# Kernel optimization log

Hardware: AMD Instinct MI355X
Metric: run time of the kernel (lower is better)

Reference implementation:

```python
import jax, jax.numpy as jnp
import numpy as np

D, H, L, V, BS = 1024, 16, 12, 50257, 2048
HD = D // H
EPS = 1e-5


def _ln(x, w, b):
    m = jnp.mean(x, -1, keepdims=True)
    v = jnp.mean(jnp.square(x - m), -1, keepdims=True)
    return (x - m) * jax.lax.rsqrt(v + EPS) * w + b


def setup_inputs() -> dict:
    key = jax.random.key(0)
    ks = jax.random.split(key, 10)
    B, T = 4, 1024
    s = 0.02
    return {
        "idx": jax.random.randint(ks[0], (B, T), 0, V),
        "targets": jax.random.randint(ks[1], (B, T), 0, V),
        "wte": s * jax.random.normal(ks[2], (V, D), jnp.float32),
        "wpe": s * jax.random.normal(ks[3], (BS, D), jnp.float32),
        "ln1_w": jnp.ones((L, D), jnp.float32),
        "ln1_b": jnp.zeros((L, D), jnp.float32),
        "qkv_w": s * jax.random.normal(ks[4], (L, D, 3 * D), jnp.float32),
        "qkv_b": jnp.zeros((L, 3 * D), jnp.float32),
        "o_w": s * jax.random.normal(ks[5], (L, D, D), jnp.float32),
        "o_b": jnp.zeros((L, D), jnp.float32),
        "ln2_w": jnp.ones((L, D), jnp.float32),
        "ln2_b": jnp.zeros((L, D), jnp.float32),
        "up_w": s * jax.random.normal(ks[6], (L, D, 4 * D), jnp.float32),
        "up_b": jnp.zeros((L, 4 * D), jnp.float32),
        "down_w": s * jax.random.normal(ks[7], (L, 4 * D, D), jnp.float32),
        "down_b": jnp.zeros((L, D), jnp.float32),
        "lnf_w": jnp.ones((D,), jnp.float32),
        "lnf_b": jnp.zeros((D,), jnp.float32),
        "lm_b": jnp.zeros((V,), jnp.float32),
    }


def _gpt(idx, targets, wte, wpe, ln1_w, ln1_b, qkv_w, qkv_b, o_w, o_b,
         ln2_w, ln2_b, up_w, up_b, down_w, down_b, lnf_w, lnf_b, lm_b):
    B, T = idx.shape
    x = wte[idx] + wpe[:T][None, :, :]  # [B,T,D]
    causal = jnp.tril(jnp.ones((T, T), bool))
    scale = HD ** -0.5

    def block(h, p):
        (l1w, l1b, qw, qb, ow, ob, l2w, l2b, uw, ub, dw, db) = p
        y = _ln(h, l1w, l1b)
        qkv = y @ qw + qb  # [B,T,3D]
        q, k, v = jnp.split(qkv, 3, axis=-1)
        q = q.reshape(B, T, H, HD)
        k = k.reshape(B, T, H, HD)
        v = v.reshape(B, T, H, HD)
        scores = jnp.einsum('bqhd,bkhd->bhqk', q, k) * scale
        scores = jnp.where(causal, scores, -jnp.inf)
        attn = jax.nn.softmax(scores, axis=-1)
        o = jnp.einsum('bhqk,bkhd->bqhd', attn, v).reshape(B, T, D)
        h = h + o @ ow + ob
        y = _ln(h, l2w, l2b)
        y = jax.nn.gelu(y @ uw + ub, approximate=False)
        h = h + y @ dw + db
        return h, None

    params = (ln1_w, ln1_b, qkv_w, qkv_b, o_w, o_b, ln2_w, ln2_b, up_w, up_b, down_w, down_b)
    x, _ = jax.lax.scan(block, x, params)
    x = _ln(x, lnf_w, lnf_b)
    logits = x @ wte.T + lm_b  # tied lm_head weight
    logp = jax.nn.log_softmax(logits, axis=-1)
    nll = -jnp.take_along_axis(logp, targets[..., None], axis=-1)[..., 0]
    loss = jnp.mean(nll)
    return logits, loss


def reference(idx, targets, wte, wpe, ln1_w, ln1_b, qkv_w, qkv_b, o_w, o_b,
              ln2_w, ln2_b, up_w, up_b, down_w, down_b, lnf_w, lnf_b, lm_b):
    return _gpt(idx, targets, wte, wpe, ln1_w, ln1_b, qkv_w, qkv_b, o_w, o_b,
                ln2_w, ln2_b, up_w, up_b, down_w, down_b, lnf_w, lnf_b, lm_b)
```

## Files before the change

### kernel.cpp

```cpp
#include <hip/hip_runtime.h>
#include <hip/hip_bf16.h>
#include <math.h>

typedef __attribute__((ext_vector_type(8))) short bfrag;
typedef __attribute__((ext_vector_type(4))) float f32x4;

static constexpr int Dm = 1024, Hh = 16, HD = 64, Ll = 12, Tt = 1024, Bb = 4;
static constexpr int Vv = 50257, Mrows = 4096;
static constexpr int PLD = 200;

__device__ inline unsigned short f2bf(float f) {
    unsigned u = __float_as_uint(f);
    u += 0x7fffu + ((u >> 16) & 1u);
    return (unsigned short)(u >> 16);
}
__device__ inline float bf2f(unsigned short s) {
    return __uint_as_float(((unsigned)s) << 16);
}

__device__ inline void gload16(const unsigned short* g, unsigned short* l) {
    __builtin_amdgcn_global_load_lds(
        (const __attribute__((address_space(1))) void*)g,
        (__attribute__((address_space(3))) void*)l, 16, 0, 0);
}

__global__ __launch_bounds__(256)
void embed_kernel(float* __restrict__ x, const float* __restrict__ wte,
                  const float* __restrict__ wpe, const int* __restrict__ idx) {
    int row = blockIdx.x;
    int t = row & (Tt - 1);
    int id = idx[row];
    int c = threadIdx.x * 4;
    float4 a = *reinterpret_cast<const float4*>(&wte[(size_t)id * Dm + c]);
    float4 p = *reinterpret_cast<const float4*>(&wpe[(size_t)t * Dm + c]);
    float4 o;
    o.x = a.x + p.x; o.y = a.y + p.y; o.z = a.z + p.z; o.w = a.w + p.w;
    *reinterpret_cast<float4*>(&x[(size_t)row * Dm + c]) = o;
}

__global__ __launch_bounds__(256)
void ln_kernel(unsigned short* __restrict__ y, const float* __restrict__ x,
               const float* __restrict__ w, const float* __restrict__ b) {
    int row = blockIdx.x;
    int tid = threadIdx.x;
    int lane = tid & 63, wv = tid >> 6;
    const float* xr = x + (size_t)row * Dm;
    float4 v = *reinterpret_cast<const float4*>(&xr[tid * 4]);
    float s1 = v.x + v.y + v.z + v.w;
    float s2 = v.x * v.x + v.y * v.y + v.z * v.z + v.w * v.w;
#pragma unroll
    for (int off = 1; off < 64; off <<= 1) {
        s1 += __shfl_xor(s1, off);
        s2 += __shfl_xor(s2, off);
    }
    __shared__ float r1[4], r2[4];
    if (lane == 0) { r1[wv] = s1; r2[wv] = s2; }
    __syncthreads();
    s1 = r1[0] + r1[1] + r1[2] + r1[3];
    s2 = r2[0] + r2[1] + r2[2] + r2[3];
    float mean = s1 * (1.0f / Dm);
    float var = s2 * (1.0f / Dm) - mean * mean;
    float rstd = rsqrtf(var + 1e-5f);
    float4 wvv = *reinterpret_cast<const float4*>(&w[tid * 4]);
    float4 bv = *reinterpret_cast<const float4*>(&b[tid * 4]);
    ushort4 o;
    o.x = f2bf((v.x - mean) * rstd * wvv.x + bv.x);
    o.y = f2bf((v.y - mean) * rstd * wvv.y + bv.y);
    o.z = f2bf((v.z - mean) * rstd * wvv.z + bv.z);
    o.w = f2bf((v.w - mean) * rstd * wvv.w + bv.w);
    *reinterpret_cast<ushort4*>(&y[(size_t)row * Dm + tid * 4]) = o;
}

__global__ __launch_bounds__(256)
void transpose_layer(const float* __restrict__ qw, const float* __restrict__ ow,
                     const float* __restrict__ uw, const float* __restrict__ dw,
                     unsigned short* __restrict__ wTq, unsigned short* __restrict__ wTo,
                     unsigned short* __restrict__ wTu, unsigned short* __restrict__ wTd) {
    __shared__ float t[32][33];
    int tb = blockIdx.x;
    const float* src; unsigned short* dst; int K, N, nx, base;
    if (tb < 3072)      { src = qw; dst = wTq; K = 1024; N = 3072; nx = 96;  base = 0; }
    else if (tb < 4096) { src = ow; dst = wTo; K = 1024; N = 1024; nx = 32;  base = 3072; }
    else if (tb < 8192) { src = uw; dst = wTu; K = 1024; N = 4096; nx = 128; base = 4096; }
    else                { src = dw; dst = wTd; K = 4096; N = 1024; nx = 32;  base = 8192; }
    int tt = tb - base;
    int n0 = (tt % nx) * 32, k0 = (tt / nx) * 32;
    int tid = threadIdx.x;
    int r = tid >> 3, c4 = (tid & 7) * 4;
    float4 v = *reinterpret_cast<const float4*>(&src[(size_t)(k0 + r) * N + n0 + c4]);
    t[r][c4] = v.x; t[r][c4 + 1] = v.y; t[r][c4 + 2] = v.z; t[r][c4 + 3] = v.w;
    __syncthreads();
    int nr = tid >> 3, kc = (tid & 7) * 4;
    ushort4 o;
    o.x = f2bf(t[kc][nr]);
    o.y = f2bf(t[kc + 1][nr]);
    o.z = f2bf(t[kc + 2][nr]);
    o.w = f2bf(t[kc + 3][nr]);
    *reinterpret_cast<ushort4*>(&dst[(size_t)(n0 + nr) * K + k0 + kc]) = o;
}

__global__ __launch_bounds__(128)
void cvt_rows(unsigned short* __restrict__ dst, const float* __restrict__ src) {
    int row = blockIdx.x;
    int t = threadIdx.x;
    const float* s = src + (size_t)row * Dm + t * 8;
    float4 f0 = *reinterpret_cast<const float4*>(s);
    float4 f1 = *reinterpret_cast<const float4*>(s + 4);
    ushort4 o0, o1;
    o0.x = f2bf(f0.x); o0.y = f2bf(f0.y); o0.z = f2bf(f0.z); o0.w = f2bf(f0.w);
    o1.x = f2bf(f1.x); o1.y = f2bf(f1.y); o1.z = f2bf(f1.z); o1.w = f2bf(f1.w);
    unsigned short* d = dst + (size_t)row * Dm + t * 8;
    *reinterpret_cast<ushort4*>(d) = o0;
    *reinterpret_cast<ushort4*>(d + 4) = o1;
}

template<int EPI, int GN>
__global__ __launch_bounds__(512, 2)
void gemm256(const unsigned short* __restrict__ A, const unsigned short* __restrict__ B,
             const float* __restrict__ bias, void* __restrict__ Cp,
             int Nv, int K, int ldc, int ncol,
             float* __restrict__ pm_out, float* __restrict__ ps_out) {
    __shared__ unsigned short As[4][256 * 32];
    __shared__ unsigned short Bs[4][256 * 32];
    const int tid = threadIdx.x;
    const int lane = tid & 63, w = tid >> 6;
    const int wr = w >> 2, wc = w & 3;
    const int g = lane >> 4, lr = lane & 15;
    const int slotk = (lr >> 1) & 3;

    const int gx = gridDim.x;
    const int ny = GN ? ((Nv + 255) >> 8) : (int)gridDim.y;
    {
    }
    int s = blockIdx.y * gx + blockIdx.x;
    int xcd = s & 7, t0 = s >> 3;
    int xblk = t0 % gx, istr = t0 / gx;
    int y = xcd + (istr << 3);
    if (GN && y >= ny) return;
    const int bm = xblk * 256;
    const int bn = y * 256;

    const int srow = lane >> 2;
    const int gsrc = (lane & 3) ^ ((lane >> 3) & 3);
    const int rA0 = (w * 2 + 0) * 16 + srow;
    const int rA1 = (w * 2 + 1) * 16 + srow;
    const size_t aoff0 = (size_t)(bm + rA0) * K + gsrc * 8;
    const size_t aoff1 = (size_t)(bm + rA1) * K + gsrc * 8;
    int gb0 = bn + rA0, gb1 = bn + rA1;
    if (GN) { gb0 = (gb0 < Nv) ? gb0 : (Nv - 1); gb1 = (gb1 < Nv) ? gb1 : (Nv - 1); }
    const size_t boff0 = (size_t)gb0 * K + gsrc * 8;
    const size_t boff1 = (size_t)gb1 * K + gsrc * 8;
    unsigned short* lA0 = &As[0][(w * 2 + 0) * 512];
    unsigned short* lA1 = &As[0][(w * 2 + 1) * 512];
    unsigned short* lB0 = &Bs[0][(w * 2 + 0) * 512];
    unsigned short* lB1 = &Bs[0][(w * 2 + 1) * 512];

    const int nt = K >> 5;

    f32x4 acc[8][4];
#pragma unroll
    for (int i = 0; i < 8; ++i)
#pragma unroll
        for (int j = 0; j < 4; ++j)
#pragma unroll
            for (int r = 0; r < 4; ++r) acc[i][j][r] = 0.f;

#pragma unroll
    for (int tp = 0; tp < 3; ++tp) {
        const int kp = tp << 5;
        gload16(A + aoff0 + kp, lA0 + tp * 8192);
        gload16(B + boff0 + kp, lB0 + tp * 8192);
        gload16(A + aoff1 + kp, lA1 + tp * 8192);
        gload16(B + boff1 + kp, lB1 + tp * 8192);
    }
    asm volatile("s_waitcnt vmcnt(8)" ::: "memory");
    asm volatile("s_barrier" ::: "memory");

    for (int t = 0; t < nt; ++t) {
        const int bt = t & 3;
        const unsigned short* as = As[bt];
        const unsigned short* bs = Bs[bt];
        const int pf = t + 3;
        const int kp = pf << 5;
        const int so = (pf & 3) * 8192;

        bfrag bfr[4], af[8];
#pragma unroll
        for (int ni = 0; ni < 4; ++ni) {
            int row = wc * 64 + ni * 16 + lr;
            bfr[ni] = *reinterpret_cast<const bfrag*>(&bs[row * 32 + ((g ^ slotk) * 8)]);
        }
#pragma unroll
        for (int mi = 0; mi < 8; ++mi) {
            int row = wr * 128 + mi * 16 + lr;
            af[mi] = *reinterpret_cast<const bfrag*>(&as[row * 32 + ((g ^ slotk) * 8)]);
        }
        if (pf < nt) {
            gload16(A + aoff0 + kp, lA0 + so);
            gload16(B + boff0 + kp, lB0 + so);
            gload16(A + aoff1 + kp, lA1 + so);
            gload16(B + boff1 + kp, lB1 + so);
        }
        __builtin_amdgcn_s_setprio(1);
#pragma unroll
        for (int mi = 0; mi < 8; ++mi)
#pragma unroll
            for (int ni = 0; ni < 4; ++ni)
                acc[mi][ni] = __builtin_amdgcn_mfma_f32_16x16x32_bf16(
                    af[mi], bfr[ni], acc[mi][ni], 0, 0, 0);
        __builtin_amdgcn_s_setprio(0);
        if (t + 3 < nt)      asm volatile("s_waitcnt vmcnt(8)" ::: "memory");
        else if (t + 2 < nt) asm volatile("s_waitcnt vmcnt(4)" ::: "memory");
        else if (t + 1 < nt) asm volatile("s_waitcnt vmcnt(0)" ::: "memory");
        asm volatile("s_barrier" ::: "memory");
    }

    unsigned short* Cb = (unsigned short*)Cp;
    float* Cf = (float*)Cp;

    if (EPI != 4) {
#pragma unroll
        for (int ni = 0; ni < 4; ++ni) {
            int col = bn + wc * 64 + ni * 16 + lr;
            if (GN && col >= Nv) continue;
            int gcol = ncol + col;
            float bi = bias[gcol];
#pragma unroll
            for (int mi = 0; mi < 8; ++mi) {
                int row0 = bm + wr * 128 + mi * 16 + g * 4;
#pragma unroll
                for (int r = 0; r < 4; ++r) {
                    int row = row0 + r;
                    float v = acc[mi][ni][r] + bi;
                    if (EPI == 0) {
                        Cb[(size_t)row * ldc + gcol] = f2bf(v);
                    } else {
                        v = 0.5f * v * (1.0f + erff(v * 0.70710678118654752f));
                        Cb[(size_t)row * ldc + gcol] = f2bf(v);
                    }
                }
            }
        }
    } else {
        __syncthreads();
        float* lm = (float*)&As[0][0];
        float* lsd = lm + 1024;
        float bi4[4];
        int colv[4];
#pragma unroll
        for (int ni = 0; ni < 4; ++ni) {
            colv[ni] = bn + wc * 64 + ni * 16 + lr;
            bi4[ni] = (colv[ni] < Nv) ? bias[ncol + colv[ni]] : 0.f;
        }
#pragma unroll
        for (int mi = 0; mi < 8; ++mi) {
#pragma unroll
            for (int r = 0; r < 4; ++r) {
                int row = bm + wr * 128 + mi * 16 + g * 4 + r;
                float vv[4];
                float ml = -3.0e38f, sl = 0.f;
#pragma unroll
                for (int ni = 0; ni < 4; ++ni) {
                    float v = acc[mi][ni][r] + bi4[ni];
                    vv[ni] = v;
                    if (colv[ni] < Nv) ml = fmaxf(ml, v);
                }
#pragma unroll
                for (int ni = 0; ni < 4; ++ni) {
                    if (colv[ni] < Nv) {
                        sl += __expf(vv[ni] - ml);
                        __builtin_nontemporal_store(
                            vv[ni], &Cf[(size_t)row * ldc + ncol + colv[ni]]);
                    }
                }
#pragma unroll
                for (int off = 1; off < 16; off <<= 1) {
                    float om = __shfl_xor(ml, off);
                    float os = __shfl_xor(sl, off);
                    float nm = fmaxf(ml, om);
                    sl = sl * __expf(ml - nm) + os * __expf(om - nm);
                    ml = nm;
                }
                if (lr == 0) {
                    int lrow = wr * 128 + mi * 16 + g * 4 + r;
                    lm[lrow * 4 + wc] = ml;
                    lsd[lrow * 4 + wc] = sl;
                }
            }
        }
        __syncthreads();
        if (tid < 256) {
            float m0 = lm[tid * 4 + 0], m1 = lm[tid * 4 + 1];
            float m2 = lm[tid * 4 + 2], m3 = lm[tid * 4 + 3];
            float M = fmaxf(fmaxf(m0, m1), fmaxf(m2, m3));
            float S = lsd[tid * 4 + 0] * __expf(m0 - M) + lsd[tid * 4 + 1] * __expf(m1 - M)
                    + lsd[tid * 4 + 2] * __expf(m2 - M) + lsd[tid * 4 + 3] * __expf(m3 - M);
            int row = bm + tid;
            int bno = bn >> 8;
            pm_out[(size_t)row * PLD + bno] = M;
            ps_out[(size_t)row * PLD + bno] = S;
        }
    }
}

template<int EPI>
__global__ __launch_bounds__(256, 2)
void gemm128p(const unsigned short* __restrict__ A, const unsigned short* __restrict__ B,
              const float* __restrict__ bias, const float* __restrict__ R,
              void* __restrict__ Cp, int K, int ldc) {
    __shared__ unsigned short As[4][128 * 32];
    __shared__ unsigned short Bs[4][128 * 32];
    const int tid = threadIdx.x;
    const int lane = tid & 63, w = tid >> 6;
    const int wr = w >> 1, wc = w & 1;
    const int g = lane >> 4, lr = lane & 15;
    const int slotk = (lr >> 1) & 3;

    const int gx = gridDim.x;
    int s = blockIdx.y * gx + blockIdx.x;
    int xcd = s & 7, t0 = s >> 3;
    int xblk = t0 % gx, istr = t0 / gx;
    int y = xcd + (istr << 3);
    const int bm = xblk * 128;
    const int bn = y * 128;

    const int srow = lane >> 2;
    const int gsrc = (lane & 3) ^ ((lane >> 3) & 3);
    const int rA0 = (w * 2 + 0) * 16 + srow;
    const int rA1 = (w * 2 + 1) * 16 + srow;
    const size_t aoff0 = (size_t)(bm + rA0) * K + gsrc * 8;
    const size_t aoff1 = (size_t)(bm + rA1) * K + gsrc * 8;
    const size_t boff0 = (size_t)(bn + rA0) * K + gsrc * 8;
    const size_t boff1 = (size_t)(bn + rA1) * K + gsrc * 8;
    unsigned short* lA0 = &As[0][(w * 2 + 0) * 512];
    unsigned short* lA1 = &As[0][(w * 2 + 1) * 512];
    unsigned short* lB0 = &Bs[0][(w * 2 + 0) * 512];
    unsigned short* lB1 = &Bs[0][(w * 2 + 1) * 512];

    const int nt = K >> 5;

    f32x4 acc[4][4];
#pragma unroll
    for (int i = 0; i < 4; ++i)
#pragma unroll
        for (int j = 0; j < 4; ++j)
#pragma unroll
            for (int r = 0; r < 4; ++r) acc[i][j][r] = 0.f;

#pragma unroll
    for (int tp = 0; tp < 3; ++tp) {
        const int kp = tp << 5;
        gload16(A + aoff0 + kp, lA0 + tp * 4096);
        gload16(B + boff0 + kp, lB0 + tp * 4096);
        gload16(A + aoff1 + kp, lA1 + tp * 4096);
        gload16(B + boff1 + kp, lB1 + tp * 4096);
    }
    asm volatile("s_waitcnt vmcnt(8)" ::: "memory");
    asm volatile("s_barrier" ::: "memory");

    for (int t = 0; t < nt; ++t) {
        const int bt = t & 3;
        const unsigned short* as = As[bt];
        const unsigned short* bs = Bs[bt];
        const int pf = t + 3;
        const int kp = pf << 5;
        const int so = (pf & 3) * 4096;

        bfrag af[4], bfr[4];
#pragma unroll
        for (int i = 0; i < 4; ++i) {
            int ra = wr * 64 + i * 16 + lr;
            af[i] = *reinterpret_cast<const bfrag*>(&as[ra * 32 + ((g ^ slotk) * 8)]);
            int rb = wc * 64 + i * 16 + lr;
            bfr[i] = *reinterpret_cast<const bfrag*>(&bs[rb * 32 + ((g ^ slotk) * 8)]);
        }
        if (pf < nt) {
            gload16(A + aoff0 + kp, lA0 + so);
            gload16(B + boff0 + kp, lB0 + so);
            gload16(A + aoff1 + kp, lA1 + so);
            gload16(B + boff1 + kp, lB1 + so);
        }
        __builtin_amdgcn_s_setprio(1);
#pragma unroll
        for (int mi = 0; mi < 4; ++mi)
#pragma unroll
            for (int ni = 0; ni < 4; ++ni)
                acc[mi][ni] = __builtin_amdgcn_mfma_f32_16x16x32_bf16(
                    af[mi], bfr[ni], acc[mi][ni], 0, 0, 0);
        __builtin_amdgcn_s_setprio(0);
        if (t + 3 < nt)      asm volatile("s_waitcnt vmcnt(8)" ::: "memory");
        else if (t + 2 < nt) asm volatile("s_waitcnt vmcnt(4)" ::: "memory");
        else if (t + 1 < nt) asm volatile("s_waitcnt vmcnt(0)" ::: "memory");
        asm volatile("s_barrier" ::: "memory");
    }

    unsigned short* Cb = (unsigned short*)Cp;
    float* Cf = (float*)Cp;
#pragma unroll
    for (int ni = 0; ni < 4; ++ni) {
        int col = bn + wc * 64 + ni * 16 + lr;
        float bi = bias[col];
#pragma unroll
        for (int mi = 0; mi < 4; ++mi) {
            int row0 = bm + wr * 64 + mi * 16 + g * 4;
#pragma unroll
            for (int r = 0; r < 4; ++r) {
                int row = row0 + r;
                float v = acc[mi][ni][r] + bi;
                if (EPI == 0) {
                    Cb[(size_t)row * ldc + col] = f2bf(v);
                } else {
                    Cf[(size_t)row * ldc + col] = R[(size_t)row * ldc + col] + v;
                }
            }
        }
    }
}

__global__ __launch_bounds__(256)
void attn_mfma(const unsigned short* __restrict__ qkv, unsigned short* __restrict__ ob) {
    const int bq = blockIdx.x;
    const int h = blockIdx.y;
    const int b = blockIdx.z;
    const int tid = threadIdx.x, lane = tid & 63, w = tid >> 6;
    const int g = lane >> 4, lr = lane & 15;
    const int qg0 = bq * 128 + w * 32;

    __shared__ unsigned short Kt[64 * 72];
    __shared__ unsigned short Vt[64 * 72];
    __shared__ unsigned short Pl[4][32 * 72];
    unsigned short* Plw = Pl[w];

    bfrag aq[2][2];
#pragma unroll
    for (int qs = 0; qs < 2; ++qs)
#pragma unroll
        for (int ks = 0; ks < 2; ++ks) {
            int row = qg0 + qs * 16 + lr;
            aq[qs][ks] = *reinterpret_cast<const bfrag*>(
                &qkv[(size_t)(b * Tt + row) * 3072 + h * 64 + ks * 32 + g * 8]);
        }

    float mrow[2][4], lrow[2][4], osc[2][4];
    f32x4 oacc[2][4];
#pragma unroll
    for (int qs = 0; qs < 2; ++qs)
#pragma unroll
        for (int r = 0; r < 4; ++r) { mrow[qs][r] = -3.0e38f; lrow[qs][r] = 0.f; }
#pragma unroll
    for (int qs = 0; qs < 2; ++qs)
#pragma unroll
        for (int dn = 0; dn < 4; ++dn)
#pragma unroll
            for (int r = 0; r < 4; ++r) oacc[qs][dn][r] = 0.f;

    const int ntile = 2 * bq + 2;
    for (int kt = 0; kt < ntile; ++kt) {
        {
            int row = tid >> 2, seg = tid & 3;
            const unsigned short* sk =
                &qkv[(size_t)(b * Tt + kt * 64 + row) * 3072 + Dm + h * 64 + seg * 16];
            bfrag kv0 = *(const bfrag*)sk;
            bfrag kv1 = *(const bfrag*)(sk + 8);
            *reinterpret_cast<bfrag*>(&Kt[row * 72 + seg * 16]) = kv0;
            *reinterpret_cast<bfrag*>(&Kt[row * 72 + seg * 16 + 8]) = kv1;
            const uint4* sv = reinterpret_cast<const uint4*>(
                &qkv[(size_t)(b * Tt + kt * 64 + row) * 3072 + 2 * Dm + h * 64 + seg * 16]);
            uint4 u0 = sv[0], u1 = sv[1];
            uint4 a, r0, r1;
            a.x = (seg & 1) ? u0.y : u0.x; a.y = (seg & 1) ? u0.z : u0.y;
            a.z = (seg & 1) ? u0.w : u0.z; a.w = (seg & 1) ? u0.x : u0.w;
            r0.x = (seg & 2) ? a.z : a.x; r0.y = (seg & 2) ? a.w : a.y;
            r0.z = (seg & 2) ? a.x : a.z; r0.w = (seg & 2) ? a.y : a.w;
            a.x = (seg & 1) ? u1.y : u1.x; a.y = (seg & 1) ? u1.z : u1.y;
            a.z = (seg & 1) ? u1.w : u1.z; a.w = (seg & 1) ? u1.x : u1.w;
            r1.x = (seg & 2) ? a.z : a.x; r1.y = (seg & 2) ? a.w : a.y;
            r1.z = (seg & 2) ? a.x : a.z; r1.w = (seg & 2) ? a.y : a.w;
            unsigned w0[4] = {r0.x, r0.y, r0.z, r0.w};
            unsigned w1[4] = {r1.x, r1.y, r1.z, r1.w};
#pragma unroll
            for (int i = 0; i < 8; ++i) {
                int j = (i + 2 * seg) & 7;
                unsigned ww = w0[i >> 1];
                unsigned short val = (i & 1) ? (unsigned short)(ww >> 16)
                                             : (unsigned short)(ww & 0xffff);
                Vt[(seg * 16 + j) * 72 + row] = val;
            }
#pragma unroll
            for (int i = 0; i < 8; ++i) {
                int j = (i + 2 * seg) & 7;
                unsigned ww = w1[i >> 1];
                unsigned short val = (i & 1) ? (unsigned short)(ww >> 16)
                                             : (unsigned short)(ww & 0xffff);
                Vt[(seg * 16 + 8 + j) * 72 + row] = val;
            }
        }
        __syncthreads();

        bool active = (kt * 64 <= qg0 + 31);
        if (active) {
            f32x4 s[2][4];
#pragma unroll
            for (int qs = 0; qs < 2; ++qs)
#pragma unroll
                for (int n = 0; n < 4; ++n)
#pragma unroll
                    for (int r = 0; r < 4; ++r) s[qs][n][r] = 0.f;
            bfrag bk[4][2];
#pragma unroll
            for (int n = 0; n < 4; ++n)
#pragma unroll
                for (int ks = 0; ks < 2; ++ks)
                    bk[n][ks] = *reinterpret_cast<const bfrag*>(
                        &Kt[(n * 16 + lr) * 72 + ks * 32 + g * 8]);
#pragma unroll
            for (int qs = 0; qs < 2; ++qs)
#pragma unroll
                for (int n = 0; n < 4; ++n)
#pragma unroll
                    for (int ks = 0; ks < 2; ++ks)
                        s[qs][n] = __builtin_amdgcn_mfma_f32_16x16x32_bf16(
                            aq[qs][ks], bk[n][ks], s[qs][n], 0, 0, 0);

            bool mayMask = (kt * 64 + 63 > qg0);
            float pv[2][4][4];
#pragma unroll
            for (int qs = 0; qs < 2; ++qs) {
#pragma unroll
                for (int r = 0; r < 4; ++r) {
                    int qrow = qg0 + qs * 16 + g * 4 + r;
                    float v[4];
#pragma unroll
                    for (int n = 0; n < 4; ++n) {
                        float sv = s[qs][n][r] * 0.125f;
                        if (mayMask && (kt * 64 + n * 16 + lr > qrow)) sv = -3.0e38f;
                        v[n] = sv;
                    }
                    float tmax = fmaxf(fmaxf(v[0], v[1]), fmaxf(v[2], v[3]));
                    tmax = fmaxf(tmax, __shfl_xor(tmax, 1));
                    tmax = fmaxf(tmax, __shfl_xor(tmax, 2));
                    tmax = fmaxf(tmax, __shfl_xor(tmax, 4));
                    tmax = fmaxf(tmax, __shfl_xor(tmax, 8));
                    float mold = mrow[qs][r];
                    float mnew = fmaxf(mold, tmax);
                    float scl = expf(mold - mnew);
                    float psum = 0.f;
#pragma unroll
                    for (int n = 0; n < 4; ++n) {
                        float p = expf(v[n] - mnew);
                        pv[qs][n][r] = p;
                        psum += p;
                    }
                    psum += __shfl_xor(psum, 1);
                    psum += __shfl_xor(psum, 2);
                    psum += __shfl_xor(psum, 4);
                    psum += __shfl_xor(psum, 8);
                    lrow[qs][r] = lrow[qs][r] * scl + psum;
                    mrow[qs][r] = mnew;
                    osc[qs][r] = scl;
                }
            }
#pragma unroll
            for (int qs = 0; qs < 2; ++qs)
#pragma unroll
                for (int dn = 0; dn < 4; ++dn)
#pragma unroll
                    for (int r = 0; r < 4; ++r) oacc[qs][dn][r] *= osc[qs][r];
#pragma unroll
            for (int qs = 0; qs < 2; ++qs)
#pragma unroll
                for (int n = 0; n < 4; ++n)
#pragma unroll
                    for (int r = 0; r < 4; ++r)
                        Plw[(qs * 16 + g * 4 + r) * 72 + n * 16 + lr] = f2bf(pv[qs][n][r]);
            asm volatile("s_waitcnt lgkmcnt(0)" ::: "memory");
            bfrag ap[2][2], bv[4][2];
#pragma unroll
            for (int qs = 0; qs < 2; ++qs)
#pragma unroll
                for (int ks = 0; ks < 2; ++ks)
                    ap[qs][ks] = *reinterpret_cast<const bfrag*>(
                        &Plw[(qs * 16 + lr) * 72 + ks * 32 + g * 8]);
#pragma unroll
            for (int dn = 0; dn < 4; ++dn)
#pragma unroll
                for (int ks = 0; ks < 2; ++ks)
                    bv[dn][ks] = *reinterpret_cast<const bfrag*>(
                        &Vt[(dn * 16 + lr) * 72 + ks * 32 + g * 8]);
#pragma unroll
            for (int qs = 0; qs < 2; ++qs)
#pragma unroll
                for (int dn = 0; dn < 4; ++dn)
#pragma unroll
                    for (int ks = 0; ks < 2; ++ks)
                        oacc[qs][dn] = __builtin_amdgcn_mfma_f32_16x16x32_bf16(
                            ap[qs][ks], bv[dn][ks], oacc[qs][dn], 0, 0, 0);
        }
        __syncthreads();
    }

#pragma unroll
    for (int qs = 0; qs < 2; ++qs)
#pragma unroll
        for (int r = 0; r < 4; ++r) {
            float rinv = 1.0f / lrow[qs][r];
            int qrow = qg0 + qs * 16 + g * 4 + r;
#pragma unroll
            for (int dn = 0; dn < 4; ++dn)
                ob[(size_t)(b * Tt + qrow) * Dm + h * 64 + dn * 16 + lr] =
                    f2bf(oacc[qs][dn][r] * rinv);
        }
}

__global__ __launch_bounds__(64)
void loss_combine(float* __restrict__ nll, const float* __restrict__ pm,
                  const float* __restrict__ ps, const float* __restrict__ logits,
                  const int* __restrict__ targets, int nby) {
    const int row = blockIdx.x;
    const int lane = threadIdx.x;
    float m = -3.0e38f, s = 0.f;
    for (int j = lane; j < nby; j += 64) {
        float om = pm[(size_t)row * PLD + j];
        float os = ps[(size_t)row * PLD + j];
        float nm = fmaxf(m, om);
        s = s * __expf(m - nm) + os * __expf(om - nm);
        m = nm;
    }
#pragma unroll
    for (int off = 1; off < 64; off <<= 1) {
        float om = __shfl_xor(m, off);
        float os = __shfl_xor(s, off);
        float nm = fmaxf(m, om);
        s = s * __expf(m - nm) + os * __expf(om - nm);
        m = nm;
    }
    if (lane == 0) {
        float lse = m + __logf(s);
        nll[row] = lse - logits[(size_t)row * Vv + targets[row]];
    }
}

__global__ __launch_bounds__(256)
void loss_reduce_kernel(float* __restrict__ loss, const float* __restrict__ nll) {
    int tid = threadIdx.x;
    __shared__ float red[256];
    float s = 0.f;
    for (int j = tid; j < Mrows; j += 256) s += nll[j];
    red[tid] = s;
    __syncthreads();
    for (int st = 128; st > 0; st >>= 1) {
        if (tid < st) red[tid] += red[tid + st];
        __syncthreads();
    }
    if (tid == 0) *loss = red[0] * (1.0f / Mrows);
}

extern "C" void kernel_launch(void* const* d_in, const int* in_sizes, int n_in,
                              void* d_out, int out_size, void* d_ws, size_t ws_size,
                              hipStream_t stream) {
    const int* idx = (const int*)d_in[0];
    const int* targets = (const int*)d_in[1];
    const float* wte = (const float*)d_in[2];
    const float* wpe = (const float*)d_in[3];
    const float* ln1_w = (const float*)d_in[4];
    const float* ln1_b = (const float*)d_in[5];
    const float* qkv_w = (const float*)d_in[6];
    const float* qkv_b = (const float*)d_in[7];
    const float* o_w = (const float*)d_in[8];
    const float* o_b = (const float*)d_in[9];
    const float* ln2_w = (const float*)d_in[10];
    const float* ln2_b = (const float*)d_in[11];
    const float* up_w = (const float*)d_in[12];
    const float* up_b = (const float*)d_in[13];
    const float* down_w = (const float*)d_in[14];
    const float* down_b = (const float*)d_in[15];
    const float* lnf_w = (const float*)d_in[16];
    const float* lnf_b = (const float*)d_in[17];
    const float* lm_b = (const float*)d_in[18];

    float* logits = (float*)d_out;
    char* ws = (char*)d_ws;
    const size_t MB = 1 << 20;
    float* x            = (float*)(ws);
    unsigned short* y   = (unsigned short*)(ws + 16 * MB);
    unsigned short* qkv = (unsigned short*)(ws + 24 * MB);
    unsigned short* ob  = (unsigned short*)(ws + 48 * MB);
    unsigned short* up  = (unsigned short*)(ws + 56 * MB);
    unsigned short* wTq = (unsigned short*)(ws + 88 * MB);
    unsigned short* wTo = (unsigned short*)(ws + 96 * MB);
    unsigned short* wTu = (unsigned short*)(ws + 100 * MB);
    unsigned short* wTd = (unsigned short*)(ws + 112 * MB);
    float* nll          = (float*)(ws + 127 * MB);
    unsigned short* wbf = (unsigned short*)(ws + 24 * MB);
    float* pmp          = (float*)(ws + 131 * MB);
    float* psp          = (float*)(ws + 136 * MB);

    embed_kernel<<<Mrows, 256, 0, stream>>>(x, wte, wpe, idx);

    for (int l = 0; l < Ll; ++l) {
        ln_kernel<<<Mrows, 256, 0, stream>>>(y, x, ln1_w + l * Dm, ln1_b + l * Dm);
        transpose_layer<<<12288, 256, 0, stream>>>(
            qkv_w + (size_t)l * Dm * 3 * Dm, o_w + (size_t)l * Dm * Dm,
            up_w + (size_t)l * Dm * 4 * Dm, down_w + (size_t)l * 4 * Dm * Dm,
            wTq, wTo, wTu, wTd);
        gemm128p<0><<<dim3(Mrows / 128, 3 * Dm / 128), 256, 0, stream>>>(
            y, wTq, qkv_b + (size_t)l * 3 * Dm, nullptr, qkv, Dm, 3 * Dm);
        attn_mfma<<<dim3(8, Hh, Bb), 256, 0, stream>>>(qkv, ob);
        gemm128p<2><<<dim3(Mrows / 128, Dm / 128), 256, 0, stream>>>(
            ob, wTo, o_b + (size_t)l * Dm, x, x, Dm, Dm);
        ln_kernel<<<Mrows, 256, 0, stream>>>(y, x, ln2_w + l * Dm, ln2_b + l * Dm);
        gemm256<1, 0><<<dim3(Mrows / 256, 4 * Dm / 256), 512, 0, stream>>>(
            y, wTu, up_b + (size_t)l * 4 * Dm, up, 4 * Dm, Dm, 4 * Dm, 0,
            nullptr, nullptr);
        gemm128p<2><<<dim3(Mrows / 128, Dm / 128), 256, 0, stream>>>(
            up, wTd, down_b + (size_t)l * Dm, x, x, 4 * Dm, Dm);
    }

    ln_kernel<<<Mrows, 256, 0, stream>>>(y, x, lnf_w, lnf_b);

    cvt_rows<<<Vv, 128, 0, stream>>>(wbf, wte);
    const int NBY = (Vv + 255) / 256;
    const int NBY_PAD = ((NBY + 7) / 8) * 8;
    gemm256<4, 1><<<dim3(Mrows / 256, NBY_PAD), 512, 0, stream>>>(
        y, wbf, lm_b, logits, Vv, Dm, Vv, 0, pmp, psp);

    loss_combine<<<Mrows, 64, 0, stream>>>(nll, pmp, psp, logits, targets, NBY);
    loss_reduce_kernel<<<1, 256, 0, stream>>>(logits + (size_t)Mrows * Vv, nll);
}
```

Baseline: 4.301 ms.

## Rewrite 256x256 GEMM as ping-pong double-buffered K=64 pipeline with split loads

Replaces the 4-stage K=32 gemm256 with gemm256p8, which uses K=64 tiles double-buffered in LDS as A/B halves. Global-to-LDS loads are interleaved across four sub-phases per tile, with barriers between MFMA groups, in the style of an 8-wave ping-pong schedule. Occupancy drops to one block per CU (launch_bounds 512,1). The aim is to amortize barrier and wait overhead and overlap loads with MFMA for the MLP up-projection and LM-head GEMMs, at the cost of more barriers and lower occupancy.

```diff
diff --git a/kernel.cpp b/kernel.cpp
--- a/kernel.cpp
+++ b/kernel.cpp
@@ -115,47 +115,45 @@
 }
 
 template<int EPI, int GN>
-__global__ __launch_bounds__(512, 2)
-void gemm256(const unsigned short* __restrict__ A, const unsigned short* __restrict__ B,
-             const float* __restrict__ bias, void* __restrict__ Cp,
-             int Nv, int K, int ldc, int ncol,
-             float* __restrict__ pm_out, float* __restrict__ ps_out) {
-    __shared__ unsigned short As[4][256 * 32];
-    __shared__ unsigned short Bs[4][256 * 32];
+__global__ __launch_bounds__(512, 1)
+void gemm256p8(const unsigned short* __restrict__ A, const unsigned short* __restrict__ B,
+               const float* __restrict__ bias, void* __restrict__ Cp,
+               int Nv, int K, int ldc, int ncol,
+               float* __restrict__ pm_out, float* __restrict__ ps_out) {
+    __shared__ unsigned short AL[2][2][8192];
+    __shared__ unsigned short BL[2][2][8192];
     const int tid = threadIdx.x;
     const int lane = tid & 63, w = tid >> 6;
     const int wr = w >> 2, wc = w & 3;
     const int g = lane >> 4, lr = lane & 15;
-    const int slotk = (lr >> 1) & 3;
 
     const int gx = gridDim.x;
     const int ny = GN ? ((Nv + 255) >> 8) : (int)gridDim.y;
-    {
-    }
     int s = blockIdx.y * gx + blockIdx.x;
-    int xcd = s & 7, t0 = s >> 3;
-    int xblk = t0 % gx, istr = t0 / gx;
+    int xcd = s & 7, t0b = s >> 3;
+    int xblk = t0b % gx, istr = t0b / gx;
     int y = xcd + (istr << 3);
     if (GN && y >= ny) return;
     const int bm = xblk * 256;
     const int bn = y * 256;
 
-    const int srow = lane >> 2;
-    const int gsrc = (lane & 3) ^ ((lane >> 3) & 3);
-    const int rA0 = (w * 2 + 0) * 16 + srow;
-    const int rA1 = (w * 2 + 1) * 16 + srow;
-    const size_t aoff0 = (size_t)(bm + rA0) * K + gsrc * 8;
-    const size_t aoff1 = (size_t)(bm + rA1) * K + gsrc * 8;
-    int gb0 = bn + rA0, gb1 = bn + rA1;
-    if (GN) { gb0 = (gb0 < Nv) ? gb0 : (Nv - 1); gb1 = (gb1 < Nv) ? gb1 : (Nv - 1); }
-    const size_t boff0 = (size_t)gb0 * K + gsrc * 8;
-    const size_t boff1 = (size_t)gb1 * K + gsrc * 8;
-    unsigned short* lA0 = &As[0][(w * 2 + 0) * 512];
-    unsigned short* lA1 = &As[0][(w * 2 + 1) * 512];
-    unsigned short* lB0 = &Bs[0][(w * 2 + 0) * 512];
-    unsigned short* lB1 = &Bs[0][(w * 2 + 1) * 512];
-
-    const int nt = K >> 5;
+    const int srow = tid >> 3;
+    const int gsrc = (tid & 7) ^ (srow & 7);
+    size_t aofs[2][2], bofs[2][2];
+#pragma unroll
+    for (int h = 0; h < 2; ++h)
+#pragma unroll
+        for (int j = 0; j < 2; ++j) {
+            int ra = bm + h * 128 + srow + j * 64;
+            aofs[h][j] = (size_t)ra * K + gsrc * 8;
+            int rb = bn + h * 128 + srow + j * 64;
+            if (GN) rb = (rb < Nv) ? rb : (Nv - 1);
+            bofs[h][j] = (size_t)rb * K + gsrc * 8;
+        }
+    const int dst0 = tid * 8, dst1 = tid * 8 + 4096;
+
+    const int nt = K >> 6;
+    const int ni = nt >> 1;
 
     f32x4 acc[8][4];
 #pragma unroll
@@ -165,64 +163,119 @@
 #pragma unroll
             for (int r = 0; r < 4; ++r) acc[i][j][r] = 0.f;
 
-#pragma unroll
-    for (int tp = 0; tp < 3; ++tp) {
-        const int kp = tp << 5;
-        gload16(A + aoff0 + kp, lA0 + tp * 8192);
-        gload16(B + boff0 + kp, lB0 + tp * 8192);
-        gload16(A + aoff1 + kp, lA1 + tp * 8192);
-        gload16(B + boff1 + kp, lB1 + tp * 8192);
-    }
-    asm volatile("s_waitcnt vmcnt(8)" ::: "memory");
+#define STG_A(d, h, kt) do { \
+        gload16(A + aofs[h][0] + ((size_t)(kt) << 6), &AL[d][h][dst0]); \
+        gload16(A + aofs[h][1] + ((size_t)(kt) << 6), &AL[d][h][dst1]); } while (0)
+#define STG_B(d, h, kt) do { \
+        gload16(B + bofs[h][0] + ((size_t)(kt) << 6), &BL[d][h][dst0]); \
+        gload16(B + bofs[h][1] + ((size_t)(kt) << 6), &BL[d][h][dst1]); } while (0)
+
+    STG_B(0, 0, 0); STG_B(0, 1, 0);
+    STG_A(0, 0, 0); STG_A(0, 1, 0);
+    STG_B(1, 0, 1); STG_B(1, 1, 1);
+    asm volatile("s_waitcnt vmcnt(0)" ::: "memory");
     asm volatile("s_barrier" ::: "memory");
 
-    for (int t = 0; t < nt; ++t) {
-        const int bt = t & 3;
-        const unsigned short* as = As[bt];
-        const unsigned short* bs = Bs[bt];
-        const int pf = t + 3;
-        const int kp = pf << 5;
-        const int so = (pf & 3) * 8192;
-
-        bfrag bfr[4], af[8];
-#pragma unroll
-        for (int ni = 0; ni < 4; ++ni) {
-            int row = wc * 64 + ni * 16 + lr;
-            bfr[ni] = *reinterpret_cast<const bfrag*>(&bs[row * 32 + ((g ^ slotk) * 8)]);
-        }
-#pragma unroll
-        for (int mi = 0; mi < 8; ++mi) {
-            int row = wr * 128 + mi * 16 + lr;
-            af[mi] = *reinterpret_cast<const bfrag*>(&as[row * 32 + ((g ^ slotk) * 8)]);
-        }
-        if (pf < nt) {
-            gload16(A + aoff0 + kp, lA0 + so);
-            gload16(B + boff0 + kp, lB0 + so);
-            gload16(A + aoff1 + kp, lA1 + so);
-            gload16(B + boff1 + kp, lB1 + so);
-        }
-        __builtin_amdgcn_s_setprio(1);
-#pragma unroll
-        for (int mi = 0; mi < 8; ++mi)
-#pragma unroll
-            for (int ni = 0; ni < 4; ++ni)
-                acc[mi][ni] = __builtin_amdgcn_mfma_f32_16x16x32_bf16(
-                    af[mi], bfr[ni], acc[mi][ni], 0, 0, 0);
-        __builtin_amdgcn_s_setprio(0);
-        if (t + 3 < nt)      asm volatile("s_waitcnt vmcnt(8)" ::: "memory");
-        else if (t + 2 < nt) asm volatile("s_waitcnt vmcnt(4)" ::: "memory");
-        else if (t + 1 < nt) asm volatile("s_waitcnt vmcnt(0)" ::: "memory");
-        asm volatile("s_barrier" ::: "memory");
-    }
+    const unsigned short* alw[2] = { &AL[0][wr][0], &AL[1][wr][0] };
+    const unsigned short* blw[2] = { &BL[0][wc >> 1][0], &BL[1][wc >> 1][0] };
+    const int rbB = (wc & 1) * 64;
+
+    bfrag bfr[4][2], afr[2][2];
+
+    for (int i = 0; i < ni; ++i) {
+        const int t1 = 2 * i + 1;
+        const int tp0 = 2 * i + 2, tp1 = 2 * i + 3;
+        const bool pf = (tp0 < nt);
+#pragma unroll
+        for (int q = 0; q < 4; ++q) {
+            if (q == 0) {
+#pragma unroll
+                for (int n_ = 0; n_ < 4; ++n_)
+#pragma unroll
+                    for (int ks = 0; ks < 2; ++ks) {
+                        int row = rbB + n_ * 16 + lr;
+                        int sg = (ks * 4 + g) ^ (row & 7);
+                        bfr[n_][ks] = *reinterpret_cast<const bfrag*>(&blw[0][row * 64 + sg * 8]);
+                    }
+            }
+#pragma unroll
+            for (int m2 = 0; m2 < 2; ++m2)
+#pragma unroll
+                for (int ks = 0; ks < 2; ++ks) {
+                    int row = q * 32 + m2 * 16 + lr;
+                    int sg = (ks * 4 + g) ^ (row & 7);
+                    afr[m2][ks] = *reinterpret_cast<const bfrag*>(&alw[0][row * 64 + sg * 8]);
+                }
+            if (q == 0)      { STG_A(1, 0, t1); }
+            else if (q == 1) { STG_A(1, 1, t1); }
+            else if (q == 2) { if (pf) STG_B(0, 0, tp0); }
+            else             { if (pf) STG_B(0, 1, tp0); }
+            asm volatile("s_barrier" ::: "memory");
+            __builtin_amdgcn_s_setprio(1);
+#pragma unroll
+            for (int m2 = 0; m2 < 2; ++m2)
+#pragma unroll
+                for (int n_ = 0; n_ < 4; ++n_)
+#pragma unroll
+                    for (int ks = 0; ks < 2; ++ks)
+                        acc[q * 2 + m2][n_] = __builtin_amdgcn_mfma_f32_16x16x32_bf16(
+                            afr[m2][ks], bfr[n_][ks], acc[q * 2 + m2][n_], 0, 0, 0);
+            __builtin_amdgcn_s_setprio(0);
+            if (q == 3) {
+                if (i + 1 < ni) asm volatile("s_waitcnt vmcnt(4)" ::: "memory");
+                else            asm volatile("s_waitcnt vmcnt(0)" ::: "memory");
+            }
+            asm volatile("s_barrier" ::: "memory");
+        }
+#pragma unroll
+        for (int q = 0; q < 4; ++q) {
+            if (q == 0) {
+#pragma unroll
+                for (int n_ = 0; n_ < 4; ++n_)
+#pragma unroll
+                    for (int ks = 0; ks < 2; ++ks) {
+                        int row = rbB + n_ * 16 + lr;
+                        int sg = (ks * 4 + g) ^ (row & 7);
+                        bfr[n_][ks] = *reinterpret_cast<const bfrag*>(&blw[1][row * 64 + sg * 8]);
+                    }
+            }
+#pragma unroll
+            for (int m2 = 0; m2 < 2; ++m2)
+#pragma unroll
+                for (int ks = 0; ks < 2; ++ks) {
+                    int row = q * 32 + m2 * 16 + lr;
+                    int sg = (ks * 4 + g) ^ (row & 7);
+                    afr[m2][ks] = *reinterpret_cast<const bfrag*>(&alw[1][row * 64 + sg * 8]);
+                }
+            if (q == 0)      { if (pf) STG_A(0, 0, tp0); }
+            else if (q == 1) { if (pf) STG_A(0, 1, tp0); }
+            else if (q == 2) { if (tp1 < nt) STG_B(1, 0, tp1); }
+            else             { if (tp1 < nt) STG_B(1, 1, tp1); }
+            asm volatile("s_barrier" ::: "memory");
+            __builtin_amdgcn_s_setprio(1);
+#pragma unroll
+            for (int m2 = 0; m2 < 2; ++m2)
+#pragma unroll
+                for (int n_ = 0; n_ < 4; ++n_)
+#pragma unroll
+                    for (int ks = 0; ks < 2; ++ks)
+                        acc[q * 2 + m2][n_] = __builtin_amdgcn_mfma_f32_16x16x32_bf16(
+                            afr[m2][ks], bfr[n_][ks], acc[q * 2 + m2][n_], 0, 0, 0);
+            __builtin_amdgcn_s_setprio(0);
+            if (q == 3 && i + 1 < ni) asm volatile("s_waitcnt vmcnt(4)" ::: "memory");
+            asm volatile("s_barrier" ::: "memory");
+        }
+    }
+#undef STG_A
+#undef STG_B
 
     unsigned short* Cb = (unsigned short*)Cp;
     float* Cf = (float*)Cp;
 
-    if (EPI != 4) {
-#pragma unroll
-        for (int ni = 0; ni < 4; ++ni) {
-            int col = bn + wc * 64 + ni * 16 + lr;
-            if (GN && col >= Nv) continue;
+    if (EPI == 1) {
+#pragma unroll
+        for (int n_ = 0; n_ < 4; ++n_) {
+            int col = bn + wc * 64 + n_ * 16 + lr;
             int gcol = ncol + col;
             float bi = bias[gcol];
 #pragma unroll
@@ -231,26 +284,22 @@
 #pragma unroll
                 for (int r = 0; r < 4; ++r) {
                     int row = row0 + r;
-                    float v = acc[mi][ni][r] + bi;
-                    if (EPI == 0) {
-                        Cb[(size_t)row * ldc + gcol] = f2bf(v);
-                    } else {
-                        v = 0.5f * v * (1.0f + erff(v * 0.70710678118654752f));
-                        Cb[(size_t)row * ldc + gcol] = f2bf(v);
-                    }
+                    float v = acc[mi][n_][r] + bi;
+                    v = 0.5f * v * (1.0f + erff(v * 0.70710678118654752f));
+                    Cb[(size_t)row * ldc + gcol] = f2bf(v);
                 }
             }
         }
     } else {
         __syncthreads();
-        float* lm = (float*)&As[0][0];
+        float* lm = (float*)&AL[0][0][0];
         float* lsd = lm + 1024;
         float bi4[4];
         int colv[4];
 #pragma unroll
-        for (int ni = 0; ni < 4; ++ni) {
-            colv[ni] = bn + wc * 64 + ni * 16 + lr;
-            bi4[ni] = (colv[ni] < Nv) ? bias[ncol + colv[ni]] : 0.f;
+        for (int n_ = 0; n_ < 4; ++n_) {
+            colv[n_] = bn + wc * 64 + n_ * 16 + lr;
+            bi4[n_] = (colv[n_] < Nv) ? bias[ncol + colv[n_]] : 0.f;
         }
 #pragma unroll
         for (int mi = 0; mi < 8; ++mi) {
@@ -260,17 +309,17 @@
                 float vv[4];
                 float ml = -3.0e38f, sl = 0.f;
 #pragma unroll
-                for (int ni = 0; ni < 4; ++ni) {
-                    float v = acc[mi][ni][r] + bi4[ni];
-                    vv[ni] = v;
-                    if (colv[ni] < Nv) ml = fmaxf(ml, v);
-                }
-#pragma unroll
-                for (int ni = 0; ni < 4; ++ni) {
-                    if (colv[ni] < Nv) {
-                        sl += __expf(vv[ni] - ml);
+                for (int n_ = 0; n_ < 4; ++n_) {
+                    float v = acc[mi][n_][r] + bi4[n_];
+                    vv[n_] = v;
+                    if (colv[n_] < Nv) ml = fmaxf(ml, v);
+                }
+#pragma unroll
+                for (int n_ = 0; n_ < 4; ++n_) {
+                    if (colv[n_] < Nv) {
+                        sl += __expf(vv[n_] - ml);
                         __builtin_nontemporal_store(
-                            vv[ni], &Cf[(size_t)row * ldc + ncol + colv[ni]]);
+                            vv[n_], &Cf[(size_t)row * ldc + ncol + colv[n_]]);
                     }
                 }
 #pragma unroll
@@ -709,7 +758,7 @@
         gemm128p<2><<<dim3(Mrows / 128, Dm / 128), 256, 0, stream>>>(
             ob, wTo, o_b + (size_t)l * Dm, x, x, Dm, Dm);
         ln_kernel<<<Mrows, 256, 0, stream>>>(y, x, ln2_w + l * Dm, ln2_b + l * Dm);
-        gemm256<1, 0><<<dim3(Mrows / 256, 4 * Dm / 256), 512, 0, stream>>>(
+        gemm256p8<1, 0><<<dim3(Mrows / 256, 4 * Dm / 256), 512, 0, stream>>>(
             y, wTu, up_b + (size_t)l * 4 * Dm, up, 4 * Dm, Dm, 4 * Dm, 0,
             nullptr, nullptr);
         gemm128p<2><<<dim3(Mrows / 128, Dm / 128), 256, 0, stream>>>(
@@ -721,7 +770,7 @@
     cvt_rows<<<Vv, 128, 0, stream>>>(wbf, wte);
     const int NBY = (Vv + 255) / 256;
     const int NBY_PAD = ((NBY + 7) / 8) * 8;
-    gemm256<4, 1><<<dim3(Mrows / 256, NBY_PAD), 512, 0, stream>>>(
+    gemm256p8<4, 1><<<dim3(Mrows / 256, NBY_PAD), 512, 0, stream>>>(
         y, wbf, lm_b, logits, Vv, Dm, Vv, 0, pmp, psp);
 
     loss_combine<<<Mrows, 64, 0, stream>>>(nll, pmp, psp, logits, targets, NBY);
```

Result: no change. 4.300 ms (median of 3 runs) (-0.0%).
